# Optimization experiments

Measured on AMD Instinct MI355X. Metric: run time of the kernel, lower is better.

## Reference

```python
import jax, jax.numpy as jnp
import numpy as np

B, C, H, L = 4, 1, 1024, 8192
KD, NS = 64, 4  # kernel_dim, num_scales


def _interp_linear(x, out_len):
    """F.interpolate(mode='linear', align_corners=False) along last axis."""
    in_len = x.shape[-1]
    if out_len == in_len:
        return x
    scale = out_len / in_len
    coord = (jnp.arange(out_len, dtype=jnp.float32) + 0.5) / scale - 0.5
    coord = jnp.clip(coord, 0.0, in_len - 1)
    lo = jnp.floor(coord).astype(jnp.int32)
    hi = jnp.minimum(lo + 1, in_len - 1)
    w = coord - lo.astype(jnp.float32)
    return x[..., lo] * (1.0 - w) + x[..., hi] * w


def setup_inputs() -> dict:
    key = jax.random.key(0)
    ks = jax.random.split(key, 8)
    u = jax.random.normal(ks[0], (B, H, L), jnp.float32)
    k0 = jax.random.normal(ks[1], (C, H, KD), jnp.float32)
    k1 = jax.random.normal(ks[2], (C, H, KD), jnp.float32)
    k2 = jax.random.normal(ks[3], (C, H, KD), jnp.float32)
    k3 = jax.random.normal(ks[4], (C, H, KD), jnp.float32)
    D = jax.random.normal(ks[5], (C, H), jnp.float32)
    W = jax.random.normal(ks[6], (H, C * H), jnp.float32) / np.float32(np.sqrt(C * H))
    b = jnp.zeros((H,), jnp.float32)
    return {"u": u, "k0": k0, "k1": k1, "k2": k2, "k3": k3, "D": D, "W": W, "b": b}


def reference(u, k0, k1, k2, k3, D, W, b):
    Lq = u.shape[-1]
    kernels = [k0, k1, k2, k3]
    total = KD * 2 ** (NS - 1)  # 512
    # multi-scale kernel build: interpolate -> right-pad -> scale -> sum
    parts = []
    for i in range(NS):
        ki = _interp_linear(kernels[i], KD * 2 ** i)
        ki = jnp.pad(ki, ((0, 0), (0, 0), (0, total - KD * 2 ** i)))
        parts.append(ki * (2.0 ** (NS - i - 1)))
    k = parts[0] + parts[1] + parts[2] + parts[3]  # (C,H,512)
    # fit to sequence length L
    if k.shape[-1] > Lq:
        k = k[..., :Lq]
    elif k.shape[-1] < Lq:
        k = jnp.pad(k, ((0, 0), (0, 0), (0, Lq - k.shape[-1])))
    # detached kernel norm
    knorm = jax.lax.stop_gradient(
        jnp.linalg.norm(k, axis=-1, keepdims=True))
    k = k / knorm
    # FFT long convolution
    n = 2 * Lq
    k_f = jnp.fft.rfft(k, n=n)              # (C,H,L+1) complex
    u_f = jnp.fft.rfft(u, n=n)              # (B,H,L+1) complex
    y_f = jnp.einsum('bhl,chl->bchl', u_f, k_f)
    y = jnp.fft.irfft(y_f, n=n)[..., :Lq]   # (B,C,H,L)
    # D skip (outer product)
    y = y + jnp.einsum('bhl,ch->bchl', u, D)
    y = y.reshape(y.shape[0], C * H, Lq)    # (B,C*H,L)
    # activation (exact gelu, torch default), dropout=Identity, norm=Identity
    y = jax.nn.gelu(y, approximate=False)
    # output_linear: 1x1 conv (C*H -> H) with bias, Identity post-activation
    y = jnp.einsum('bfl,of->bol', y, W) + b[None, :, None]
    return y
```

## Files before the change

kernel.cpp:

```cpp
#include <hip/hip_runtime.h>
#include <cstdint>
#include <cstddef>

#define HH 1024
#define LL 8192
#define NB 4
#define KD 64
#define KLEN 512
#define LHALF 4096

typedef float v4f  __attribute__((ext_vector_type(4)));
typedef float v16f __attribute__((ext_vector_type(16)));
typedef short v8s  __attribute__((ext_vector_type(8)));

__device__ __forceinline__ unsigned short f2bf(float f) {
  union { float f; unsigned int u; } x; x.f = f;
  unsigned int r = x.u + 0x7fffu + ((x.u >> 16) & 1u);
  return (unsigned short)(r >> 16);
}

__device__ __forceinline__ float bfbits2f(unsigned int hi16) {
  union { unsigned int u; float f; } x; x.u = hi16;
  return x.f;
}

__device__ __forceinline__ float gelu_f(float y) {
  float x = y * 0.70710678118654752f;
  float ax = fabsf(x);
  float t = __builtin_amdgcn_rcpf(fmaf(0.3275911f, ax, 1.0f));
  float p = t * fmaf(t, fmaf(t, fmaf(t, fmaf(t, 1.061405429f, -1.453152027f),
                                     1.421413741f), -0.284496736f), 0.254829592f);
  float e = __expf(-x * x);
  float erfax = fmaf(-p, e, 1.0f);
  float er = copysignf(erfax, x);
  return 0.5f * y * (1.0f + er);
}

__global__ __launch_bounds__(512) void build_k_kernel(
    const float* __restrict__ k0, const float* __restrict__ k1,
    const float* __restrict__ k2, const float* __restrict__ k3,
    float* __restrict__ kout) {
  __shared__ float lk[4][KD];
  __shared__ float red[512];
  const int h = blockIdx.x;
  const int t = threadIdx.x;
  if (t < 256) {
    int i = t >> 6, j = t & 63;
    const float* src = (i == 0) ? k0 : (i == 1) ? k1 : (i == 2) ? k2 : k3;
    lk[i][j] = src[h * KD + j];
  }
  __syncthreads();
  float kt = 0.f;
#pragma unroll
  for (int i = 0; i < 4; i++) {
    int len = KD << i;
    if (t < len) {
      float inv = 1.0f / (float)(1 << i);
      float c = ((float)t + 0.5f) * inv - 0.5f;
      c = fminf(fmaxf(c, 0.0f), 63.0f);
      int lo = (int)floorf(c);
      int hi = min(lo + 1, 63);
      float w = c - (float)lo;
      float v = lk[i][lo] * (1.0f - w) + lk[i][hi] * w;
      kt += v * (float)(1 << (3 - i));
    }
  }
  red[t] = kt * kt;
  __syncthreads();
  for (int s = 256; s > 0; s >>= 1) {
    if (t < s) red[t] += red[t + s];
    __syncthreads();
  }
  float norm = sqrtf(red[0]);
  kout[h * KLEN + t] = kt / norm;
}

__global__ void w2bf_kernel(const float* __restrict__ W,
                            unsigned short* __restrict__ Wb, int n) {
  int i = blockIdx.x * blockDim.x + threadIdx.x;
  if (i < n) Wb[i] = f2bf(W[i]);
}

__device__ __forceinline__ int suswz(int b) { return b ^ (((b >> 7) & 3) << 4); }

__global__ __launch_bounds__(256) void conv_kernel(
    const float* __restrict__ u, const float* __restrict__ kk,
    const float* __restrict__ D, unsigned short* __restrict__ g) {
  __shared__ __align__(16) unsigned short Apk[34 * 512];
  __shared__ __align__(16) unsigned short su[512 + LHALF];
  __shared__ __align__(16) float skk[KLEN];

  const int bid = blockIdx.x;
  const int h = bid >> 1;
  const int half = bid & 1;
  const int l0 = half * LHALF;
  const int tid = threadIdx.x;
  const int w = tid >> 6;
  const int ln = tid & 63;
  const int n = ln & 31;
  const int q = ln >> 5;
  char* sub = (char*)su;

  if (tid < 128) *(float4*)(skk + tid * 4) = *(const float4*)(kk + (size_t)h * KLEN + tid * 4);
  __syncthreads();

#pragma unroll 4
  for (int e = 0; e < 68; ++e) {
    int idx = e * 256 + tid;
    int s = idx >> 9;
    int lane = (idx >> 3) & 63;
    int j = idx & 7;
    int m = lane & 31, q2 = lane >> 5;
    int c = ((s & 1) << 4) + (q2 << 3) + j;
    int t = ((s >> 1) << 5) + m - c;
    Apk[idx] = (t >= 0 && t < KLEN) ? f2bf(skk[t]) : (unsigned short)0;
  }

  const float Dh = D[h];
  const int bbyte0 = 1024 + 64 * (w * 32 + n) + 16 * q;

  for (int b = 0; b < NB; ++b) {
    __syncthreads();
    const float* __restrict__ urow = u + ((size_t)b * HH + h) * LL;
    if (tid < 128) {
      int i = tid * 4;
      uint2 p;
      if (half == 0) {
        p.x = 0u; p.y = 0u;
      } else {
        float4 v = *(const float4*)(urow + l0 - 512 + i);
        p.x = (unsigned)f2bf(v.x) | ((unsigned)f2bf(v.y) << 16);
        p.y = (unsigned)f2bf(v.z) | ((unsigned)f2bf(v.w) << 16);
      }
      *(uint2*)(sub + suswz(2 * i)) = p;
    }
#pragma unroll
    for (int r = 0; r < 4; ++r) {
      int i = r * 1024 + tid * 4;
      float4 v = *(const float4*)(urow + l0 + i);
      uint2 p;
      p.x = (unsigned)f2bf(v.x) | ((unsigned)f2bf(v.y) << 16);
      p.y = (unsigned)f2bf(v.z) | ((unsigned)f2bf(v.w) << 16);
      *(uint2*)(sub + suswz(1024 + 2 * i)) = p;
    }
    __syncthreads();

    v16f acc;
#pragma unroll
    for (int r = 0; r < 16; ++r) acc[r] = 0.f;

#pragma unroll
    for (int s = 0; s < 34; ++s) {
      const int offb = ((s & 1) << 5) - ((s >> 1) << 6);
      v8s af = *(const v8s*)(Apk + (s << 9) + (ln << 3));
      v8s b0 = *(const v8s*)(sub + suswz(bbyte0 + offb));
      acc = __builtin_amdgcn_mfma_f32_32x32x16_bf16(af, b0, acc, 0, 0, 0);
    }

    unsigned short* grow = g + ((size_t)b * HH + h) * LL + l0;
#pragma unroll
    for (int rg = 0; rg < 4; ++rg) {
      const int l = 32 * (w * 32 + n) + 8 * rg + 4 * q;
      uint2 up2 = *(const uint2*)(sub + suswz(1024 + 2 * l));
      float uf[4];
      uf[0] = bfbits2f(up2.x << 16);
      uf[1] = bfbits2f(up2.x & 0xffff0000u);
      uf[2] = bfbits2f(up2.y << 16);
      uf[3] = bfbits2f(up2.y & 0xffff0000u);
      unsigned short hb[4];
#pragma unroll
      for (int rr = 0; rr < 4; ++rr) {
        float y = acc[rg * 4 + rr] + Dh * uf[rr];
        hb[rr] = f2bf(gelu_f(y));
      }
      uint2 p;
      p.x = (unsigned)hb[0] | ((unsigned)hb[1] << 16);
      p.y = (unsigned)hb[2] | ((unsigned)hb[3] << 16);
      *(uint2*)(grow + l) = p;
    }
  }
}

__device__ __forceinline__ void gll16(const void* g, void* l) {
  __builtin_amdgcn_global_load_lds(
      (const __attribute__((address_space(1))) unsigned int*)g,
      (__attribute__((address_space(3))) unsigned int*)l, 16, 0, 0);
}

__global__ __launch_bounds__(256) void gemm_kernel(
    const unsigned short* __restrict__ A,
    const unsigned short* __restrict__ G,
    const float* __restrict__ bias, float* __restrict__ out) {
  __shared__ __align__(16) unsigned short sA[2][4096];
  __shared__ __align__(16) unsigned int   sB[2][2048];
  const int tid = threadIdx.x;
  const int wv = tid >> 6, ln = tid & 63;

  const int bid0 = blockIdx.x;
  const int swz = (bid0 & 7) * 256 + (bid0 >> 3);
  const int mt = swz & 7, nt = swz >> 3;
  const int o0 = mt * 128;
  const int bb = nt >> 6;
  const int l0 = (nt & 63) * 128;
  const int m16 = ln & 15, q4 = ln >> 4;
  const int wm = wv & 1, wn = wv >> 1;

  v4f acc[4][4];
#pragma unroll
  for (int i = 0; i < 4; i++)
#pragma unroll
    for (int j = 0; j < 4; j++) {
      v4f z = {0.f, 0.f, 0.f, 0.f};
      acc[i][j] = z;
    }

  const unsigned short* gA[2];
  int lA[2];
  {
    const int cc = (((ln & 3) ^ ((ln >> 3) & 3)) << 3);
#pragma unroll
    for (int qq = 0; qq < 2; qq++) {
      const int c = wv * 2 + qq;
      const int rr = c * 16 + (ln >> 2);
      gA[qq] = A + (size_t)(o0 + rr) * HH + cc;
      lA[qq] = c * 512;
    }
  }

  const int pr = tid >> 4, seg = tid & 15;
  const unsigned short* gB0 = G + ((size_t)bb * HH + 2 * pr) * LL + l0 + seg * 8;
  const unsigned short* gB1 = gB0 + LL;
  int wby[8];
#pragma unroll
  for (int e = 0; e < 8; e++) {
    int l = seg * 8 + e;
    int byi = (pr >> 2) * 2048 + l * 16 + (pr & 3) * 4;
    wby[e] = byi ^ (((l >> 3) & 7) << 4);
  }

  int aby[4], bby[4];
#pragma unroll
  for (int i = 0; i < 4; i++) {
    int row = wm * 64 + i * 16 + m16;
    aby[i] = (row * 64 + q4 * 16) ^ (((m16 >> 1) & 3) << 4);
  }
#pragma unroll
  for (int j = 0; j < 4; j++) {
    int l = wn * 64 + j * 16 + m16;
    bby[j] = (q4 * 2048 + l * 16) ^ (((l >> 3) & 7) << 4);
  }

  auto stageA = [&](int buf, int kbase) {
#pragma unroll
    for (int qq = 0; qq < 2; qq++) gll16(gA[qq] + kbase, &sA[buf][lA[qq]]);
  };
  auto packB = [&](int buf, const uint4& r0, const uint4& r1) {
    union { uint4 u; unsigned short s[8]; } ua, ub; ua.u = r0; ub.u = r1;
    char* base = (char*)sB[buf];
#pragma unroll
    for (int e = 0; e < 8; e++) {
      unsigned v = (unsigned)ua.s[e] | ((unsigned)ub.s[e] << 16);
      *(unsigned*)(base + wby[e]) = v;
    }
  };

  uint4 p0, p1, c0, c1;
  stageA(0, 0);
  __builtin_amdgcn_sched_barrier(0);
  p0 = *(const uint4*)(gB0); p1 = *(const uint4*)(gB1);
  __builtin_amdgcn_sched_barrier(0);
  c0 = *(const uint4*)(gB0 + (size_t)32 * LL);
  c1 = *(const uint4*)(gB1 + (size_t)32 * LL);
  __builtin_amdgcn_sched_barrier(0);
  packB(0, p0, p1);
  asm volatile("s_waitcnt vmcnt(2) lgkmcnt(0)" ::: "memory");
  __builtin_amdgcn_s_barrier();

  for (int kk = 0; kk < 30; ++kk) {
    const int p = kk & 1;
    v8s af[4], bf4[4];
    const char* ab = (const char*)sA[p];
    const char* bbc = (const char*)sB[p];
#pragma unroll
    for (int i = 0; i < 4; i++) af[i] = *(const v8s*)(ab + aby[i]);
#pragma unroll
    for (int j = 0; j < 4; j++) bf4[j] = *(const v8s*)(bbc + bby[j]);
    stageA(p ^ 1, (kk + 1) * 32);
    __builtin_amdgcn_sched_barrier(0);
    uint4 n0 = *(const uint4*)(gB0 + (size_t)(kk + 2) * 32 * LL);
    uint4 n1 = *(const uint4*)(gB1 + (size_t)(kk + 2) * 32 * LL);
    asm volatile("s_waitcnt lgkmcnt(0)" ::: "memory");
    __builtin_amdgcn_sched_barrier(0);
    __builtin_amdgcn_s_setprio(1);
#pragma unroll
    for (int i = 0; i < 4; i++)
#pragma unroll
      for (int j = 0; j < 4; j++)
        acc[i][j] = __builtin_amdgcn_mfma_f32_16x16x32_bf16(af[i], bf4[j], acc[i][j], 0, 0, 0);
    __builtin_amdgcn_s_setprio(0);
    asm volatile("s_waitcnt vmcnt(4)" ::: "memory");
    packB(p ^ 1, c0, c1);
    c0 = n0; c1 = n1;
    asm volatile("s_waitcnt vmcnt(2) lgkmcnt(0)" ::: "memory");
    __builtin_amdgcn_s_barrier();
  }

  {
    v8s af[4], bf4[4];
    const char* ab = (const char*)sA[0];
    const char* bbc = (const char*)sB[0];
#pragma unroll
    for (int i = 0; i < 4; i++) af[i] = *(const v8s*)(ab + aby[i]);
#pragma unroll
    for (int j = 0; j < 4; j++) bf4[j] = *(const v8s*)(bbc + bby[j]);
    stageA(1, 31 * 32);
    asm volatile("s_waitcnt lgkmcnt(0)" ::: "memory");
    __builtin_amdgcn_sched_barrier(0);
    __builtin_amdgcn_s_setprio(1);
#pragma unroll
    for (int i = 0; i < 4; i++)
#pragma unroll
      for (int j = 0; j < 4; j++)
        acc[i][j] = __builtin_amdgcn_mfma_f32_16x16x32_bf16(af[i], bf4[j], acc[i][j], 0, 0, 0);
    __builtin_amdgcn_s_setprio(0);
    asm volatile("s_waitcnt vmcnt(2)" ::: "memory");
    packB(1, c0, c1);
    asm volatile("s_waitcnt vmcnt(0) lgkmcnt(0)" ::: "memory");
    __builtin_amdgcn_s_barrier();
  }
  {
    v8s af[4], bf4[4];
    const char* ab = (const char*)sA[1];
    const char* bbc = (const char*)sB[1];
#pragma unroll
    for (int i = 0; i < 4; i++) af[i] = *(const v8s*)(ab + aby[i]);
#pragma unroll
    for (int j = 0; j < 4; j++) bf4[j] = *(const v8s*)(bbc + bby[j]);
    asm volatile("s_waitcnt lgkmcnt(0)" ::: "memory");
    __builtin_amdgcn_sched_barrier(0);
    __builtin_amdgcn_s_setprio(1);
#pragma unroll
    for (int i = 0; i < 4; i++)
#pragma unroll
      for (int j = 0; j < 4; j++)
        acc[i][j] = __builtin_amdgcn_mfma_f32_16x16x32_bf16(af[i], bf4[j], acc[i][j], 0, 0, 0);
    __builtin_amdgcn_s_setprio(0);
  }

#pragma unroll
  for (int i = 0; i < 4; i++) {
    const int ob = o0 + wm * 64 + i * 16 + q4 * 4;
#pragma unroll
    for (int j = 0; j < 4; j++) {
      const int l = l0 + wn * 64 + j * 16 + m16;
#pragma unroll
      for (int r = 0; r < 4; r++) {
        const int o = ob + r;
        out[((size_t)bb * HH + o) * LL + l] = acc[i][j][r] + bias[o];
      }
    }
  }
}

extern "C" void kernel_launch(void* const* d_in, const int* in_sizes, int n_in,
                              void* d_out, int out_size, void* d_ws, size_t ws_size,
                              hipStream_t stream) {
  const float* u   = (const float*)d_in[0];
  const float* k0  = (const float*)d_in[1];
  const float* k1  = (const float*)d_in[2];
  const float* k2  = (const float*)d_in[3];
  const float* k3  = (const float*)d_in[4];
  const float* D   = (const float*)d_in[5];
  const float* W   = (const float*)d_in[6];
  const float* bia = (const float*)d_in[7];
  float* out = (float*)d_out;

  char* ws = (char*)d_ws;
  unsigned short* g  = (unsigned short*)ws;
  float* kws         = (float*)(ws + (size_t)67108864);
  unsigned short* Wb = (unsigned short*)(ws + (size_t)69206016);

  build_k_kernel<<<HH, 512, 0, stream>>>(k0, k1, k2, k3, kws);
  w2bf_kernel<<<(HH * HH + 255) / 256, 256, 0, stream>>>(W, Wb, HH * HH);
  conv_kernel<<<HH * 2, 256, 0, stream>>>(u, kws, D, g);
  gemm_kernel<<<8 * 256, 256, 0, stream>>>(Wb, g, bia, out);
}
```

Before: 375.4 us.

## Fuse kernel build into conv and shrink GEMM N-tile to 64 for occupancy

Result: slower. 390.0 us (+3.9%).

```diff
diff --git a/kernel.cpp b/kernel.cpp
--- a/kernel.cpp
+++ b/kernel.cpp
@@ -36,45 +36,6 @@
   return 0.5f * y * (1.0f + er);
 }
 
-__global__ __launch_bounds__(512) void build_k_kernel(
-    const float* __restrict__ k0, const float* __restrict__ k1,
-    const float* __restrict__ k2, const float* __restrict__ k3,
-    float* __restrict__ kout) {
-  __shared__ float lk[4][KD];
-  __shared__ float red[512];
-  const int h = blockIdx.x;
-  const int t = threadIdx.x;
-  if (t < 256) {
-    int i = t >> 6, j = t & 63;
-    const float* src = (i == 0) ? k0 : (i == 1) ? k1 : (i == 2) ? k2 : k3;
-    lk[i][j] = src[h * KD + j];
-  }
-  __syncthreads();
-  float kt = 0.f;
-#pragma unroll
-  for (int i = 0; i < 4; i++) {
-    int len = KD << i;
-    if (t < len) {
-      float inv = 1.0f / (float)(1 << i);
-      float c = ((float)t + 0.5f) * inv - 0.5f;
-      c = fminf(fmaxf(c, 0.0f), 63.0f);
-      int lo = (int)floorf(c);
-      int hi = min(lo + 1, 63);
-      float w = c - (float)lo;
-      float v = lk[i][lo] * (1.0f - w) + lk[i][hi] * w;
-      kt += v * (float)(1 << (3 - i));
-    }
-  }
-  red[t] = kt * kt;
-  __syncthreads();
-  for (int s = 256; s > 0; s >>= 1) {
-    if (t < s) red[t] += red[t + s];
-    __syncthreads();
-  }
-  float norm = sqrtf(red[0]);
-  kout[h * KLEN + t] = kt / norm;
-}
-
 __global__ void w2bf_kernel(const float* __restrict__ W,
                             unsigned short* __restrict__ Wb, int n) {
   int i = blockIdx.x * blockDim.x + threadIdx.x;
@@ -84,11 +45,15 @@
 __device__ __forceinline__ int suswz(int b) { return b ^ (((b >> 7) & 3) << 4); }
 
 __global__ __launch_bounds__(256) void conv_kernel(
-    const float* __restrict__ u, const float* __restrict__ kk,
-    const float* __restrict__ D, unsigned short* __restrict__ g) {
+    const float* __restrict__ k0, const float* __restrict__ k1,
+    const float* __restrict__ k2, const float* __restrict__ k3,
+    const float* __restrict__ u, const float* __restrict__ D,
+    unsigned short* __restrict__ g) {
   __shared__ __align__(16) unsigned short Apk[34 * 512];
   __shared__ __align__(16) unsigned short su[512 + LHALF];
   __shared__ __align__(16) float skk[KLEN];
+  __shared__ float lk[4][KD];
+  __shared__ float sred[4];
 
   const int bid = blockIdx.x;
   const int h = bid >> 1;
@@ -101,8 +66,36 @@
   const int q = ln >> 5;
   char* sub = (char*)su;
 
-  if (tid < 128) *(float4*)(skk + tid * 4) = *(const float4*)(kk + (size_t)h * KLEN + tid * 4);
+  {
+    int i = tid >> 6, j = tid & 63;
+    const float* src = (i == 0) ? k0 : (i == 1) ? k1 : (i == 2) ? k2 : k3;
+    lk[i][j] = src[h * KD + j];
+  }
   __syncthreads();
+  float ss = 0.f;
+  for (int tt = tid; tt < KLEN; tt += 256) {
+    float kt = 0.f;
+#pragma unroll
+    for (int i = 0; i < 4; i++) {
+      int len = KD << i;
+      if (tt < len) {
+        float inv = 1.0f / (float)(1 << i);
+        float c = ((float)tt + 0.5f) * inv - 0.5f;
+        c = fminf(fmaxf(c, 0.0f), 63.0f);
+        int lo = (int)floorf(c);
+        int hi = min(lo + 1, 63);
+        float wq = c - (float)lo;
+        kt += (lk[i][lo] * (1.0f - wq) + lk[i][hi] * wq) * (float)(1 << (3 - i));
+      }
+    }
+    skk[tt] = kt;
+    ss += kt * kt;
+  }
+#pragma unroll
+  for (int off = 32; off > 0; off >>= 1) ss += __shfl_xor(ss, off);
+  if (ln == 0) sred[w] = ss;
+  __syncthreads();
+  const float invn = 1.0f / sqrtf(sred[0] + sred[1] + sred[2] + sred[3]);
 
 #pragma unroll 4
   for (int e = 0; e < 68; ++e) {
@@ -113,7 +106,7 @@
     int m = lane & 31, q2 = lane >> 5;
     int c = ((s & 1) << 4) + (q2 << 3) + j;
     int t = ((s >> 1) << 5) + m - c;
-    Apk[idx] = (t >= 0 && t < KLEN) ? f2bf(skk[t]) : (unsigned short)0;
+    Apk[idx] = (t >= 0 && t < KLEN) ? f2bf(skk[t] * invn) : (unsigned short)0;
   }
 
   const float Dh = D[h];
@@ -187,29 +180,29 @@
       (__attribute__((address_space(3))) unsigned int*)l, 16, 0, 0);
 }
 
-__global__ __launch_bounds__(256) void gemm_kernel(
+__global__ __launch_bounds__(256, 4) void gemm_kernel(
     const unsigned short* __restrict__ A,
     const unsigned short* __restrict__ G,
     const float* __restrict__ bias, float* __restrict__ out) {
   __shared__ __align__(16) unsigned short sA[2][4096];
-  __shared__ __align__(16) unsigned int   sB[2][2048];
+  __shared__ __align__(16) unsigned int   sB[2][1024];
   const int tid = threadIdx.x;
   const int wv = tid >> 6, ln = tid & 63;
 
   const int bid0 = blockIdx.x;
-  const int swz = (bid0 & 7) * 256 + (bid0 >> 3);
+  const int swz = (bid0 & 7) * 512 + (bid0 >> 3);
   const int mt = swz & 7, nt = swz >> 3;
   const int o0 = mt * 128;
-  const int bb = nt >> 6;
-  const int l0 = (nt & 63) * 128;
+  const int bb = nt >> 7;
+  const int l0 = (nt & 127) * 64;
   const int m16 = ln & 15, q4 = ln >> 4;
   const int wm = wv & 1, wn = wv >> 1;
 
-  v4f acc[4][4];
+  v4f acc[4][2];
 #pragma unroll
   for (int i = 0; i < 4; i++)
 #pragma unroll
-    for (int j = 0; j < 4; j++) {
+    for (int j = 0; j < 2; j++) {
       v4f z = {0.f, 0.f, 0.f, 0.f};
       acc[i][j] = z;
     }
@@ -227,27 +220,21 @@
     }
   }
 
-  const int pr = tid >> 4, seg = tid & 15;
+  const int pr = tid >> 3;
+  const int seg = tid & 7;
   const unsigned short* gB0 = G + ((size_t)bb * HH + 2 * pr) * LL + l0 + seg * 8;
   const unsigned short* gB1 = gB0 + LL;
-  int wby[8];
-#pragma unroll
-  for (int e = 0; e < 8; e++) {
-    int l = seg * 8 + e;
-    int byi = (pr >> 2) * 2048 + l * 16 + (pr & 3) * 4;
-    wby[e] = byi ^ (((l >> 3) & 7) << 4);
-  }
-
-  int aby[4], bby[4];
+
+  int aby[4], bby[2];
 #pragma unroll
   for (int i = 0; i < 4; i++) {
     int row = wm * 64 + i * 16 + m16;
     aby[i] = (row * 64 + q4 * 16) ^ (((m16 >> 1) & 3) << 4);
   }
 #pragma unroll
-  for (int j = 0; j < 4; j++) {
-    int l = wn * 64 + j * 16 + m16;
-    bby[j] = (q4 * 2048 + l * 16) ^ (((l >> 3) & 7) << 4);
+  for (int j = 0; j < 2; j++) {
+    int l = wn * 32 + j * 16 + m16;
+    bby[j] = (l * 64 + q4 * 16) ^ (((l >> 3) & 3) << 5);
   }
 
   auto stageA = [&](int buf, int kbase) {
@@ -259,60 +246,72 @@
     char* base = (char*)sB[buf];
 #pragma unroll
     for (int e = 0; e < 8; e++) {
+      int l = seg * 8 + e;
       unsigned v = (unsigned)ua.s[e] | ((unsigned)ub.s[e] << 16);
-      *(unsigned*)(base + wby[e]) = v;
+      *(unsigned*)(base + ((l * 64 + pr * 4) ^ ((seg & 3) << 5))) = v;
     }
   };
 
-  uint4 p0, p1, c0, c1;
+  uint4 c0, c1;
   stageA(0, 0);
   __builtin_amdgcn_sched_barrier(0);
-  p0 = *(const uint4*)(gB0); p1 = *(const uint4*)(gB1);
-  __builtin_amdgcn_sched_barrier(0);
-  c0 = *(const uint4*)(gB0 + (size_t)32 * LL);
-  c1 = *(const uint4*)(gB1 + (size_t)32 * LL);
-  __builtin_amdgcn_sched_barrier(0);
-  packB(0, p0, p1);
-  asm volatile("s_waitcnt vmcnt(2) lgkmcnt(0)" ::: "memory");
+  if (wv < 2) {
+    uint4 p0 = *(const uint4*)(gB0);
+    uint4 p1 = *(const uint4*)(gB1);
+    c0 = *(const uint4*)(gB0 + (size_t)32 * LL);
+    c1 = *(const uint4*)(gB1 + (size_t)32 * LL);
+    packB(0, p0, p1);
+    asm volatile("s_waitcnt vmcnt(2)" ::: "memory");
+  } else {
+    asm volatile("s_waitcnt vmcnt(0)" ::: "memory");
+  }
+  asm volatile("s_waitcnt lgkmcnt(0)" ::: "memory");
   __builtin_amdgcn_s_barrier();
 
   for (int kk = 0; kk < 30; ++kk) {
     const int p = kk & 1;
-    v8s af[4], bf4[4];
+    v8s af[4], bf[2];
     const char* ab = (const char*)sA[p];
     const char* bbc = (const char*)sB[p];
 #pragma unroll
     for (int i = 0; i < 4; i++) af[i] = *(const v8s*)(ab + aby[i]);
 #pragma unroll
-    for (int j = 0; j < 4; j++) bf4[j] = *(const v8s*)(bbc + bby[j]);
+    for (int j = 0; j < 2; j++) bf[j] = *(const v8s*)(bbc + bby[j]);
     stageA(p ^ 1, (kk + 1) * 32);
     __builtin_amdgcn_sched_barrier(0);
-    uint4 n0 = *(const uint4*)(gB0 + (size_t)(kk + 2) * 32 * LL);
-    uint4 n1 = *(const uint4*)(gB1 + (size_t)(kk + 2) * 32 * LL);
+    uint4 n0, n1;
+    if (wv < 2) {
+      n0 = *(const uint4*)(gB0 + (size_t)(kk + 2) * 32 * LL);
+      n1 = *(const uint4*)(gB1 + (size_t)(kk + 2) * 32 * LL);
+    }
     asm volatile("s_waitcnt lgkmcnt(0)" ::: "memory");
     __builtin_amdgcn_sched_barrier(0);
     __builtin_amdgcn_s_setprio(1);
 #pragma unroll
     for (int i = 0; i < 4; i++)
 #pragma unroll
-      for (int j = 0; j < 4; j++)
-        acc[i][j] = __builtin_amdgcn_mfma_f32_16x16x32_bf16(af[i], bf4[j], acc[i][j], 0, 0, 0);
+      for (int j = 0; j < 2; j++)
+        acc[i][j] = __builtin_amdgcn_mfma_f32_16x16x32_bf16(af[i], bf[j], acc[i][j], 0, 0, 0);
     __builtin_amdgcn_s_setprio(0);
-    asm volatile("s_waitcnt vmcnt(4)" ::: "memory");
-    packB(p ^ 1, c0, c1);
-    c0 = n0; c1 = n1;
-    asm volatile("s_waitcnt vmcnt(2) lgkmcnt(0)" ::: "memory");
+    if (wv < 2) {
+      asm volatile("s_waitcnt vmcnt(4)" ::: "memory");
+      packB(p ^ 1, c0, c1);
+      c0 = n0; c1 = n1;
+      asm volatile("s_waitcnt vmcnt(2) lgkmcnt(0)" ::: "memory");
+    } else {
+      asm volatile("s_waitcnt vmcnt(0) lgkmcnt(0)" ::: "memory");
+    }
     __builtin_amdgcn_s_barrier();
   }
 
   {
-    v8s af[4], bf4[4];
+    v8s af[4], bf[2];
     const char* ab = (const char*)sA[0];
     const char* bbc = (const char*)sB[0];
 #pragma unroll
     for (int i = 0; i < 4; i++) af[i] = *(const v8s*)(ab + aby[i]);
 #pragma unroll
-    for (int j = 0; j < 4; j++) bf4[j] = *(const v8s*)(bbc + bby[j]);
+    for (int j = 0; j < 2; j++) bf[j] = *(const v8s*)(bbc + bby[j]);
     stageA(1, 31 * 32);
     asm volatile("s_waitcnt lgkmcnt(0)" ::: "memory");
     __builtin_amdgcn_sched_barrier(0);
@@ -320,30 +319,32 @@
 #pragma unroll
     for (int i = 0; i < 4; i++)
 #pragma unroll
-      for (int j = 0; j < 4; j++)
-        acc[i][j] = __builtin_amdgcn_mfma_f32_16x16x32_bf16(af[i], bf4[j], acc[i][j], 0, 0, 0);
+      for (int j = 0; j < 2; j++)
+        acc[i][j] = __builtin_amdgcn_mfma_f32_16x16x32_bf16(af[i], bf[j], acc[i][j], 0, 0, 0);
     __builtin_amdgcn_s_setprio(0);
-    asm volatile("s_waitcnt vmcnt(2)" ::: "memory");
-    packB(1, c0, c1);
+    if (wv < 2) {
+      asm volatile("s_waitcnt vmcnt(2)" ::: "memory");
+      packB(1, c0, c1);
+    }
     asm volatile("s_waitcnt vmcnt(0) lgkmcnt(0)" ::: "memory");
     __builtin_amdgcn_s_barrier();
   }
   {
-    v8s af[4], bf4[4];
+    v8s af[4], bf[2];
     const char* ab = (const char*)sA[1];
     const char* bbc = (const char*)sB[1];
 #pragma unroll
     for (int i = 0; i < 4; i++) af[i] = *(const v8s*)(ab + aby[i]);
 #pragma unroll
-    for (int j = 0; j < 4; j++) bf4[j] = *(const v8s*)(bbc + bby[j]);
+    for (int j = 0; j < 2; j++) bf[j] = *(const v8s*)(bbc + bby[j]);
     asm volatile("s_waitcnt lgkmcnt(0)" ::: "memory");
     __builtin_amdgcn_sched_barrier(0);
     __builtin_amdgcn_s_setprio(1);
 #pragma unroll
     for (int i = 0; i < 4; i++)
 #pragma unroll
-      for (int j = 0; j < 4; j++)
-        acc[i][j] = __builtin_amdgcn_mfma_f32_16x16x32_bf16(af[i], bf4[j], acc[i][j], 0, 0, 0);
+      for (int j = 0; j < 2; j++)
+        acc[i][j] = __builtin_amdgcn_mfma_f32_16x16x32_bf16(af[i], bf[j], acc[i][j], 0, 0, 0);
     __builtin_amdgcn_s_setprio(0);
   }
 
@@ -351,8 +352,8 @@
   for (int i = 0; i < 4; i++) {
     const int ob = o0 + wm * 64 + i * 16 + q4 * 4;
 #pragma unroll
-    for (int j = 0; j < 4; j++) {
-      const int l = l0 + wn * 64 + j * 16 + m16;
+    for (int j = 0; j < 2; j++) {
+      const int l = l0 + wn * 32 + j * 16 + m16;
 #pragma unroll
       for (int r = 0; r < 4; r++) {
         const int o = ob + r;
@@ -377,11 +378,9 @@
 
   char* ws = (char*)d_ws;
   unsigned short* g  = (unsigned short*)ws;
-  float* kws         = (float*)(ws + (size_t)67108864);
-  unsigned short* Wb = (unsigned short*)(ws + (size_t)69206016);
-
-  build_k_kernel<<<HH, 512, 0, stream>>>(k0, k1, k2, k3, kws);
+  unsigned short* Wb = (unsigned short*)(ws + (size_t)67108864);
+
   w2bf_kernel<<<(HH * HH + 255) / 256, 256, 0, stream>>>(W, Wb, HH * HH);
-  conv_kernel<<<HH * 2, 256, 0, stream>>>(u, kws, D, g);
-  gemm_kernel<<<8 * 256, 256, 0, stream>>>(Wb, g, bia, out);
-}
+  conv_kernel<<<HH * 2, 256, 0, stream>>>(k0, k1, k2, k3, u, D, g);
+  gemm_kernel<<<8 * 512, 256, 0, stream>>>(Wb, g, bia, out);
+}
```
